# Kernel optimization log

Hardware: AMD Instinct MI355X
Metric: run time of the kernel (lower is better)

Reference implementation:

```python
import jax, jax.numpy as jnp
import numpy as np

B, T, DYN, STAT, H, OUT = 128, 2048, 8, 24, 256, 1

def setup_inputs() -> dict:
    key = jax.random.key(0)
    ks = jax.random.split(key, 20)
    s = lambda k, shape, fan_in: jax.random.uniform(k, shape, jnp.float32, -1.0, 1.0) / np.sqrt(fan_in)
    return {
        "x":    jax.random.normal(ks[0], (B, T, DYN + STAT), jnp.float32),
        "c0":   jax.random.normal(ks[1], (H,), jnp.float32),
        "h0":   jax.random.normal(ks[2], (H,), jnp.float32),
        "Wi":   s(ks[3], (H, STAT), STAT), "bi":   s(ks[4], (H,), STAT),
        "Wf_x": s(ks[5], (H, DYN), DYN),  "bf_x": s(ks[6], (H,), DYN),
        "Wf_h": s(ks[7], (H, H), H),      "bf_h": s(ks[8], (H,), H),
        "Wg_x": s(ks[9], (H, DYN), DYN),  "bg_x": s(ks[10], (H,), DYN),
        "Wg_h": s(ks[11], (H, H), H),     "bg_h": s(ks[12], (H,), H),
        "Wo_x": s(ks[13], (H, DYN), DYN), "bo_x": s(ks[14], (H,), DYN),
        "Wo_h": s(ks[15], (H, H), H),     "bo_h": s(ks[16], (H,), H),
        "Wout": s(ks[17], (OUT, H), H),   "bout": s(ks[18], (OUT,), H),
    }

def reference(x, c0, h0, Wi, bi, Wf_x, bf_x, Wf_h, bf_h,
              Wg_x, bg_x, Wg_h, bg_h, Wo_x, bo_x, Wo_h, bo_h, Wout, bout):
    xd = x[..., :DYN]   # [B,T,DYN] dynamic features
    xs = x[..., DYN:]   # [B,T,STAT] static features (recomputed each step, as in source)
    # Hoist all input-dependent gate pre-activations out of the recurrence.
    I  = jax.nn.sigmoid(jnp.einsum('btd,hd->bth', xs, Wi) + bi)   # input gate (static only)
    Fx = jnp.einsum('btd,hd->bth', xd, Wf_x) + bf_x
    Gx = jnp.einsum('btd,hd->bth', xd, Wg_x) + bg_x
    Ox = jnp.einsum('btd,hd->bth', xd, Wo_x) + bo_x

    def step(carry, inp):
        c, h = carry
        i_t, fx, gx, ox = inp
        f = jax.nn.sigmoid(fx + h @ Wf_h.T + bf_h)
        g = jnp.tanh(gx + h @ Wg_h.T + bg_h)
        o = jax.nn.sigmoid(ox + h @ Wo_h.T + bo_h)
        out = o @ Wout.T + bout          # NOTE: source computes output from o_t (pre-update)
        c = f * c + i_t * g
        h = o * jnp.tanh(c)
        return (c, h), out

    carry0 = (jnp.broadcast_to(c0, (B, H)), jnp.broadcast_to(h0, (B, H)))
    seq = (jnp.swapaxes(I, 0, 1), jnp.swapaxes(Fx, 0, 1),
           jnp.swapaxes(Gx, 0, 1), jnp.swapaxes(Ox, 0, 1))  # [T,B,H] each
    _, outs = jax.lax.scan(step, carry0, seq)
    return jnp.swapaxes(outs, 0, 1)  # [B,T,OUT]
```

## Files before the change

kernel.cpp:

```cpp
#include <hip/hip_runtime.h>
#include <hip/hip_bf16.h>


#define T_LEN 2048
#define HD 256

typedef __attribute__((ext_vector_type(8))) short bf16x8;
typedef __attribute__((ext_vector_type(4))) float f32x4;

#define LOG2E 1.4426950408889634f

__device__ __forceinline__ short f2bf(float f) {
  unsigned u = __float_as_uint(f);
  unsigned r = (u + 0x7fffu + ((u >> 16) & 1u)) >> 16;
  return (short)r;
}

__device__ __forceinline__ bf16x8 loadw8(const float* p) {
  bf16x8 r;
#pragma unroll
  for (int i = 0; i < 8; ++i) r[i] = f2bf(p[i]);
  return r;
}

__device__ __forceinline__ float sigm(float x) {
  float e = __builtin_amdgcn_exp2f(-LOG2E * x);
  return __builtin_amdgcn_rcpf(1.0f + e);
}

__device__ __forceinline__ float tanh_(float x) {
  float e = __builtin_amdgcn_exp2f((2.0f * LOG2E) * x);
  return 1.0f - 2.0f * __builtin_amdgcn_rcpf(e + 1.0f);
}

__device__ __forceinline__ void wg_barrier_lgkm() {
  asm volatile("s_waitcnt lgkmcnt(0)" ::: "memory");
  __builtin_amdgcn_s_barrier();
  __builtin_amdgcn_sched_barrier(0);
}

#define ASTR 296
#define ABUF (16 * ASTR)

__global__ __launch_bounds__(512, 2) void ealstm_kernel(
    const float* __restrict__ x, const float* __restrict__ c0, const float* __restrict__ h0,
    const float* __restrict__ Wi, const float* __restrict__ bi,
    const float* __restrict__ Wfx, const float* __restrict__ bfx,
    const float* __restrict__ Wfh, const float* __restrict__ bfh,
    const float* __restrict__ Wgx, const float* __restrict__ bgx,
    const float* __restrict__ Wgh, const float* __restrict__ bgh,
    const float* __restrict__ Wox, const float* __restrict__ box_,
    const float* __restrict__ Woh, const float* __restrict__ boh,
    const float* __restrict__ Wout, const float* __restrict__ bout,
    float* __restrict__ out)
{
  __shared__ __attribute__((aligned(16))) short A_sh[2 * ABUF];
  __shared__ __attribute__((aligned(16))) short Bx_sh[8 * 8 * 512];
  __shared__ __attribute__((aligned(16))) short Bo7_sh[8 * 2 * 512];
  __shared__ float out_part[2][4][32];

  const int tid = threadIdx.x;
  const int w   = tid >> 6;
  const int l   = tid & 63;
  const int lr  = l & 15;
  const int lg  = l >> 4;
  const int n0  = w * 32;
  const int wg  = blockIdx.x;
  const bool xstage = (tid >= 384);

  bf16x8 Bf[8][2], Bg[8][2], Bo[7][2];
#pragma unroll
  for (int ks = 0; ks < 8; ++ks) {
#pragma unroll
    for (int nt = 0; nt < 2; ++nt) {
      const int n = n0 + nt * 16 + lr;
      const int k = ks * 32 + lg * 8;
      Bf[ks][nt] = loadw8(Wfh + n * HD + k);
      Bg[ks][nt] = loadw8(Wgh + n * HD + k);
      if (ks < 7) Bo[ks][nt] = loadw8(Woh + n * HD + k);
    }
  }

  short* bo7 = Bo7_sh + w * 1024;
#pragma unroll
  for (int nt = 0; nt < 2; ++nt) {
    const int n = n0 + nt * 16 + lr;
    bf16x8 fr = loadw8(Woh + n * HD + 7 * 32 + lg * 8);
    *reinterpret_cast<bf16x8*>(bo7 + nt * 512 + l * 8) = fr;
  }
  short* bxw = Bx_sh + w * 4096;
  {
    bf16x8 z = (bf16x8)(short)0;
    const float* WxArr[3] = {Wfx, Wgx, Wox};
#pragma unroll
    for (int nt = 0; nt < 2; ++nt) {
      const int n = n0 + nt * 16 + lr;
#pragma unroll
      for (int g = 0; g < 3; ++g) {
        bf16x8 fr = (lg == 0) ? loadw8(WxArr[g] + n * 8) : z;
        *reinterpret_cast<bf16x8*>(bxw + (g * 2 + nt) * 512 + l * 8) = fr;
      }
      bf16x8 fi = (lg >= 1) ? loadw8(Wi + n * 24 + (lg - 1) * 8) : z;
      *reinterpret_cast<bf16x8*>(bxw + (6 + nt) * 512 + l * 8) = fi;
    }
  }

  float bias[4][2], woutv[2], cst[2];
#pragma unroll
  for (int nt = 0; nt < 2; ++nt) {
    const int n = n0 + nt * 16 + lr;
    bias[0][nt] = bfx[n] + bfh[n];
    bias[1][nt] = bgx[n] + bgh[n];
    bias[2][nt] = box_[n] + boh[n];
    bias[3][nt] = bi[n];
    woutv[nt] = Wout[n];
    cst[nt] = c0[n];
  }
  const float boutv = bout[0];

  for (int idx = tid; idx < 2 * ABUF; idx += 512) A_sh[idx] = 0;
  __syncthreads();
  for (int idx = tid; idx < 4 * 256; idx += 512) {
    A_sh[(4 * (idx >> 8)) * ASTR + (idx & 255)] = f2bf(h0[idx & 255]);
  }
  if (xstage) {
    const int row = (tid >> 5) & 3, k = tid & 31;
    A_sh[(4 * row) * ASTR + 256 + k] = f2bf(x[((size_t)(wg * 4 + row) * T_LEN) * 32 + k]);
  }
  __syncthreads();

  const float* xp = x + (size_t)(wg * 4 + ((tid >> 5) & 3)) * T_LEN * 32 + (tid & 31);
  const int akoff = lg * 8;
  const f32x4 z4 = {0.f, 0.f, 0.f, 0.f};

  for (int t = 0; t < T_LEN; ++t) {
    const int cur = t & 1;
    const short* ArowC = A_sh + cur * ABUF + lr * ASTR;
    short* Anxt = A_sh + (cur ^ 1) * ABUF;

    if (t > 0 && w == 0 && l < 4) {
      float s = boutv;
#pragma unroll
      for (int ww = 0; ww < 32; ++ww) s += out_part[cur ^ 1][l][ww];
      out[(size_t)(wg * 4 + l) * T_LEN + (t - 1)] = s;
    }

    float xval = 0.0f;
    if (xstage) {
      const int tn = (t + 1 < T_LEN) ? (t + 1) : (T_LEN - 1);
      xval = xp[(size_t)tn * 32];
    }

    f32x4 acc[4][2];
    const bf16x8 a0 = *reinterpret_cast<const bf16x8*>(ArowC + 0 * 32 + akoff);
    const bf16x8 a1 = *reinterpret_cast<const bf16x8*>(ArowC + 1 * 32 + akoff);
    const bf16x8 a2 = *reinterpret_cast<const bf16x8*>(ArowC + 2 * 32 + akoff);
    const bf16x8 a3 = *reinterpret_cast<const bf16x8*>(ArowC + 3 * 32 + akoff);
    __builtin_amdgcn_s_setprio(1);
    {
      acc[0][0] = __builtin_amdgcn_mfma_f32_16x16x32_bf16(a0, Bf[0][0], z4, 0, 0, 0);
      acc[0][1] = __builtin_amdgcn_mfma_f32_16x16x32_bf16(a0, Bf[0][1], z4, 0, 0, 0);
      acc[1][0] = __builtin_amdgcn_mfma_f32_16x16x32_bf16(a0, Bg[0][0], z4, 0, 0, 0);
      acc[1][1] = __builtin_amdgcn_mfma_f32_16x16x32_bf16(a0, Bg[0][1], z4, 0, 0, 0);
      acc[2][0] = __builtin_amdgcn_mfma_f32_16x16x32_bf16(a0, Bo[0][0], z4, 0, 0, 0);
      acc[2][1] = __builtin_amdgcn_mfma_f32_16x16x32_bf16(a0, Bo[0][1], z4, 0, 0, 0);
    }
    {
      const bf16x8 aa[3] = {a1, a2, a3};
#pragma unroll
      for (int ks = 1; ks < 4; ++ks) {
        const bf16x8 a = aa[ks - 1];
        acc[0][0] = __builtin_amdgcn_mfma_f32_16x16x32_bf16(a, Bf[ks][0], acc[0][0], 0, 0, 0);
        acc[0][1] = __builtin_amdgcn_mfma_f32_16x16x32_bf16(a, Bf[ks][1], acc[0][1], 0, 0, 0);
        acc[1][0] = __builtin_amdgcn_mfma_f32_16x16x32_bf16(a, Bg[ks][0], acc[1][0], 0, 0, 0);
        acc[1][1] = __builtin_amdgcn_mfma_f32_16x16x32_bf16(a, Bg[ks][1], acc[1][1], 0, 0, 0);
        acc[2][0] = __builtin_amdgcn_mfma_f32_16x16x32_bf16(a, Bo[ks][0], acc[2][0], 0, 0, 0);
        acc[2][1] = __builtin_amdgcn_mfma_f32_16x16x32_bf16(a, Bo[ks][1], acc[2][1], 0, 0, 0);
      }
    }
#pragma unroll
    for (int ks = 4; ks < 8; ++ks) {
      const bf16x8 a = *reinterpret_cast<const bf16x8*>(ArowC + ks * 32 + akoff);
      acc[0][0] = __builtin_amdgcn_mfma_f32_16x16x32_bf16(a, Bf[ks][0], acc[0][0], 0, 0, 0);
      acc[0][1] = __builtin_amdgcn_mfma_f32_16x16x32_bf16(a, Bf[ks][1], acc[0][1], 0, 0, 0);
      acc[1][0] = __builtin_amdgcn_mfma_f32_16x16x32_bf16(a, Bg[ks][0], acc[1][0], 0, 0, 0);
      acc[1][1] = __builtin_amdgcn_mfma_f32_16x16x32_bf16(a, Bg[ks][1], acc[1][1], 0, 0, 0);
      if (ks < 7) {
        acc[2][0] = __builtin_amdgcn_mfma_f32_16x16x32_bf16(a, Bo[ks][0], acc[2][0], 0, 0, 0);
        acc[2][1] = __builtin_amdgcn_mfma_f32_16x16x32_bf16(a, Bo[ks][1], acc[2][1], 0, 0, 0);
      } else {
        const bf16x8 b0 = *reinterpret_cast<const bf16x8*>(bo7 + 0 * 512 + l * 8);
        const bf16x8 b1 = *reinterpret_cast<const bf16x8*>(bo7 + 1 * 512 + l * 8);
        acc[2][0] = __builtin_amdgcn_mfma_f32_16x16x32_bf16(a, b0, acc[2][0], 0, 0, 0);
        acc[2][1] = __builtin_amdgcn_mfma_f32_16x16x32_bf16(a, b1, acc[2][1], 0, 0, 0);
      }
    }
    {
      const bf16x8 ax = *reinterpret_cast<const bf16x8*>(ArowC + 256 + akoff);
#pragma unroll
      for (int g = 0; g < 3; ++g) {
#pragma unroll
        for (int nt = 0; nt < 2; ++nt) {
          const bf16x8 b = *reinterpret_cast<const bf16x8*>(bxw + (g * 2 + nt) * 512 + l * 8);
          acc[g][nt] = __builtin_amdgcn_mfma_f32_16x16x32_bf16(ax, b, acc[g][nt], 0, 0, 0);
        }
      }
#pragma unroll
      for (int nt = 0; nt < 2; ++nt) {
        const bf16x8 b = *reinterpret_cast<const bf16x8*>(bxw + (6 + nt) * 512 + l * 8);
        f32x4 cb; cb[0] = bias[3][nt]; cb[1] = bias[3][nt]; cb[2] = bias[3][nt]; cb[3] = bias[3][nt];
        acc[3][nt] = __builtin_amdgcn_mfma_f32_16x16x32_bf16(ax, b, cb, 0, 0, 0);
      }
    }
    __builtin_amdgcn_s_setprio(0);

    float po = 0.0f;
    short hpk[2];
#pragma unroll
    for (int nt = 0; nt < 2; ++nt) {
      const float fpre = acc[0][nt][0] + bias[0][nt];
      const float gpre = acc[1][nt][0] + bias[1][nt];
      const float opre = acc[2][nt][0] + bias[2][nt];
      const float ipre = acc[3][nt][0];
      const float sf = sigm(fpre);
      const float tg = tanh_(gpre);
      const float so = sigm(opre);
      const float si = sigm(ipre);
      const float c  = sf * cst[nt] + si * tg;
      cst[nt] = c;
      const float hv = so * tanh_(c);
      hpk[nt] = f2bf(hv);
      po += so * woutv[nt];
    }

    Anxt[(4 * lg) * ASTR + (n0 + lr)]      = hpk[0];
    Anxt[(4 * lg) * ASTR + (n0 + 16 + lr)] = hpk[1];
    if (xstage) Anxt[(4 * ((tid >> 5) & 3)) * ASTR + 256 + (tid & 31)] = f2bf(xval);

    po += __shfl_xor(po, 1, 64);
    po += __shfl_xor(po, 2, 64);
    if ((lr & 3) == 0) out_part[cur][lg][w * 4 + (lr >> 2)] = po;

    wg_barrier_lgkm();
  }

  if (w == 0 && l < 4) {
    float s = boutv;
#pragma unroll
    for (int ww = 0; ww < 32; ++ww) s += out_part[(T_LEN - 1) & 1][l][ww];
    out[(size_t)(wg * 4 + l) * T_LEN + (T_LEN - 1)] = s;
  }
}

extern "C" void kernel_launch(void* const* d_in, const int* in_sizes, int n_in,
                              void* d_out, int out_size, void* d_ws, size_t ws_size,
                              hipStream_t stream) {
  const float* x    = (const float*)d_in[0];
  const float* c0   = (const float*)d_in[1];
  const float* h0   = (const float*)d_in[2];
  const float* Wi   = (const float*)d_in[3];
  const float* bi   = (const float*)d_in[4];
  const float* Wfx  = (const float*)d_in[5];
  const float* bfx  = (const float*)d_in[6];
  const float* Wfh  = (const float*)d_in[7];
  const float* bfh  = (const float*)d_in[8];
  const float* Wgx  = (const float*)d_in[9];
  const float* bgx  = (const float*)d_in[10];
  const float* Wgh  = (const float*)d_in[11];
  const float* bgh  = (const float*)d_in[12];
  const float* Wox  = (const float*)d_in[13];
  const float* box_ = (const float*)d_in[14];
  const float* Woh  = (const float*)d_in[15];
  const float* boh  = (const float*)d_in[16];
  const float* Wout = (const float*)d_in[17];
  const float* bout = (const float*)d_in[18];

  ealstm_kernel<<<dim3(32), dim3(512), 0, stream>>>(
      x, c0, h0, Wi, bi, Wfx, bfx, Wfh, bfh,
      Wgx, bgx, Wgh, bgh, Wox, box_, Woh, boh, Wout, bout,
      (float*)d_out);
}
```

Before: 2.806 ms.

## Precompute input-gate pre-activations in chunks to workspace before recurrence

Adds a new kernel that, per time chunk, runs a batched MFMA pass over x to compute the input-projection gate pre-activations (with biases and sigmoid of the input gate). It stores them as packed bf16 in the workspace, and the recurrent loop then reads them through a two-step-ahead register prefetch. This removes the per-step x MFMAs, the x staging into shared memory and the associated extra A-tile columns from the serial critical path. In exchange it adds global round-trips and rounds the gate pre-activations to bf16. It falls back to the old kernel when the workspace is too small.

```diff
diff --git a/kernel.cpp b/kernel.cpp
--- a/kernel.cpp
+++ b/kernel.cpp
@@ -7,6 +7,7 @@
 
 typedef __attribute__((ext_vector_type(8))) short bf16x8;
 typedef __attribute__((ext_vector_type(4))) float f32x4;
+typedef __attribute__((ext_vector_type(4))) unsigned int u32x4;
 
 #define LOG2E 1.4426950408889634f
 
@@ -23,6 +24,15 @@
   return r;
 }
 
+__device__ __forceinline__ bf16x8 loadw8v(const float* p) {
+  const float4 v0 = *reinterpret_cast<const float4*>(p);
+  const float4 v1 = *reinterpret_cast<const float4*>(p + 4);
+  bf16x8 r;
+  r[0] = f2bf(v0.x); r[1] = f2bf(v0.y); r[2] = f2bf(v0.z); r[3] = f2bf(v0.w);
+  r[4] = f2bf(v1.x); r[5] = f2bf(v1.y); r[6] = f2bf(v1.z); r[7] = f2bf(v1.w);
+  return r;
+}
+
 __device__ __forceinline__ float sigm(float x) {
   float e = __builtin_amdgcn_exp2f(-LOG2E * x);
   return __builtin_amdgcn_rcpf(1.0f + e);
@@ -31,6 +41,11 @@
 __device__ __forceinline__ float tanh_(float x) {
   float e = __builtin_amdgcn_exp2f((2.0f * LOG2E) * x);
   return 1.0f - 2.0f * __builtin_amdgcn_rcpf(e + 1.0f);
+}
+
+__device__ __forceinline__ float punp16(u32x4 p, int idx) {
+  unsigned d = p[idx >> 1];
+  return __uint_as_float((idx & 1) ? (d & 0xffff0000u) : (d << 16));
 }
 
 __device__ __forceinline__ void wg_barrier_lgkm() {
@@ -39,10 +54,230 @@
   __builtin_amdgcn_sched_barrier(0);
 }
 
-#define ASTR 296
+#define ASTR 264
 #define ABUF (16 * ASTR)
 
-__global__ __launch_bounds__(512, 2) void ealstm_kernel(
+__global__ __launch_bounds__(512, 2) void ealstm_pp(
+    const float* __restrict__ x, const float* __restrict__ c0, const float* __restrict__ h0,
+    const float* __restrict__ Wi, const float* __restrict__ bi,
+    const float* __restrict__ Wfx, const float* __restrict__ bfx,
+    const float* __restrict__ Wfh, const float* __restrict__ bfh,
+    const float* __restrict__ Wgx, const float* __restrict__ bgx,
+    const float* __restrict__ Wgh, const float* __restrict__ bgh,
+    const float* __restrict__ Wox, const float* __restrict__ box_,
+    const float* __restrict__ Woh, const float* __restrict__ boh,
+    const float* __restrict__ Wout, const float* __restrict__ bout,
+    float* __restrict__ out, unsigned short* __restrict__ P, int tc)
+{
+  __shared__ __attribute__((aligned(16))) short A_sh[2 * ABUF];
+  __shared__ __attribute__((aligned(16))) short Bo7_sh[8 * 2 * 512];
+  __shared__ float out_part[2][4][32];
+
+  const int tid = threadIdx.x;
+  const int w   = tid >> 6;
+  const int l   = tid & 63;
+  const int lr  = l & 15;
+  const int lg  = l >> 4;
+  const int n0  = w * 32;
+  const int wg  = blockIdx.x;
+
+  bf16x8 Bw[4][2];
+  float cb[4][2];
+  {
+    bf16x8 z = (bf16x8)(short)0;
+#pragma unroll
+    for (int nt = 0; nt < 2; ++nt) {
+      const int n = n0 + nt * 16 + lr;
+      Bw[0][nt] = (lg == 0) ? loadw8(Wfx + n * 8) : z;
+      Bw[1][nt] = (lg == 0) ? loadw8(Wgx + n * 8) : z;
+      Bw[2][nt] = (lg == 0) ? loadw8(Wox + n * 8) : z;
+      Bw[3][nt] = (lg >= 1) ? loadw8(Wi + n * 24 + (lg - 1) * 8) : z;
+      cb[0][nt] = bfx[n] + bfh[n];
+      cb[1][nt] = bgx[n] + bgh[n];
+      cb[2][nt] = box_[n] + boh[n];
+      cb[3][nt] = bi[n];
+    }
+  }
+
+  bf16x8 Bf[8][2], Bg[8][2], Bo[7][2];
+#pragma unroll
+  for (int ks = 0; ks < 8; ++ks) {
+#pragma unroll
+    for (int nt = 0; nt < 2; ++nt) {
+      const int n = n0 + nt * 16 + lr;
+      const int k = ks * 32 + lg * 8;
+      Bf[ks][nt] = loadw8(Wfh + n * HD + k);
+      Bg[ks][nt] = loadw8(Wgh + n * HD + k);
+      if (ks < 7) Bo[ks][nt] = loadw8(Woh + n * HD + k);
+    }
+  }
+  short* bo7 = Bo7_sh + w * 1024;
+#pragma unroll
+  for (int nt = 0; nt < 2; ++nt) {
+    const int n = n0 + nt * 16 + lr;
+    bf16x8 fr = loadw8(Woh + n * HD + 7 * 32 + lg * 8);
+    *reinterpret_cast<bf16x8*>(bo7 + nt * 512 + l * 8) = fr;
+  }
+
+  float woutv[2], cst[2];
+#pragma unroll
+  for (int nt = 0; nt < 2; ++nt) {
+    const int n = n0 + nt * 16 + lr;
+    woutv[nt] = Wout[n];
+    cst[nt]   = c0[n];
+  }
+  const float boutv = bout[0];
+
+  for (int idx = tid; idx < 2 * ABUF; idx += 512) A_sh[idx] = 0;
+  __syncthreads();
+  for (int idx = tid; idx < 4 * 256; idx += 512) {
+    A_sh[(4 * (idx >> 8)) * ASTR + (idx & 255)] = f2bf(h0[idx & 255]);
+  }
+  __syncthreads();
+
+  unsigned short* Pw = P + ((size_t)wg * 8 + w) * ((size_t)tc * 512);
+  const unsigned short* Pr = Pw + ((size_t)lg * 16 + lr) * 8;
+  const int akoff = lg * 8;
+  const f32x4 z4 = {0.f, 0.f, 0.f, 0.f};
+
+  for (int t0c = 0; t0c < T_LEN; t0c += tc) {
+    const int ntiles = tc >> 2;
+#pragma unroll 1
+    for (int tile = 0; tile < ntiles; ++tile) {
+      const int row  = tile & 3;
+      const int trow = (tile >> 2) << 4;
+      const float* xr = x + ((size_t)(wg * 4 + row) * T_LEN + t0c + trow + lr) * 32 + akoff;
+      const bf16x8 a = loadw8v(xr);
+      f32x4 acc[4][2];
+#pragma unroll
+      for (int g = 0; g < 4; ++g) {
+#pragma unroll
+        for (int nt = 0; nt < 2; ++nt) {
+          f32x4 cbs; cbs[0] = cb[g][nt]; cbs[1] = cb[g][nt]; cbs[2] = cb[g][nt]; cbs[3] = cb[g][nt];
+          acc[g][nt] = __builtin_amdgcn_mfma_f32_16x16x32_bf16(a, Bw[g][nt], cbs, 0, 0, 0);
+        }
+      }
+#pragma unroll
+      for (int r = 0; r < 4; ++r) {
+        bf16x8 pk;
+        pk[0] = f2bf(acc[0][0][r]); pk[1] = f2bf(acc[0][1][r]);
+        pk[2] = f2bf(acc[1][0][r]); pk[3] = f2bf(acc[1][1][r]);
+        pk[4] = f2bf(acc[2][0][r]); pk[5] = f2bf(acc[2][1][r]);
+        pk[6] = f2bf(sigm(acc[3][0][r])); pk[7] = f2bf(sigm(acc[3][1][r]));
+        *reinterpret_cast<bf16x8*>(Pw + ((size_t)(trow + lg * 4 + r) * 4 + row) * 128 + lr * 8) = pk;
+      }
+    }
+    asm volatile("s_waitcnt vmcnt(0)" ::: "memory");
+
+    u32x4 pc = *reinterpret_cast<const u32x4*>(Pr);
+    u32x4 pn = *reinterpret_cast<const u32x4*>(Pr + ((tc > 1) ? 512 : 0));
+
+#pragma unroll 1
+    for (int tl = 0; tl < tc; ++tl) {
+      const int t   = t0c + tl;
+      const int cur = t & 1;
+      const short* ArowC = A_sh + cur * ABUF + lr * ASTR;
+      short* Anxt = A_sh + (cur ^ 1) * ABUF;
+
+      const int t2 = (tl + 2 < tc) ? (tl + 2) : (tc - 1);
+      const u32x4 p2 = *reinterpret_cast<const u32x4*>(Pr + (size_t)t2 * 512);
+
+      if (t > 0 && w == 0 && l < 4) {
+        float s = boutv;
+#pragma unroll
+        for (int ww = 0; ww < 32; ++ww) s += out_part[cur ^ 1][l][ww];
+        out[(size_t)(wg * 4 + l) * T_LEN + (t - 1)] = s;
+      }
+
+      f32x4 acc[3][2];
+      const bf16x8 a0 = *reinterpret_cast<const bf16x8*>(ArowC + 0 * 32 + akoff);
+      const bf16x8 a1 = *reinterpret_cast<const bf16x8*>(ArowC + 1 * 32 + akoff);
+      const bf16x8 a2 = *reinterpret_cast<const bf16x8*>(ArowC + 2 * 32 + akoff);
+      const bf16x8 a3 = *reinterpret_cast<const bf16x8*>(ArowC + 3 * 32 + akoff);
+      __builtin_amdgcn_s_setprio(1);
+      {
+        acc[0][0] = __builtin_amdgcn_mfma_f32_16x16x32_bf16(a0, Bf[0][0], z4, 0, 0, 0);
+        acc[0][1] = __builtin_amdgcn_mfma_f32_16x16x32_bf16(a0, Bf[0][1], z4, 0, 0, 0);
+        acc[1][0] = __builtin_amdgcn_mfma_f32_16x16x32_bf16(a0, Bg[0][0], z4, 0, 0, 0);
+        acc[1][1] = __builtin_amdgcn_mfma_f32_16x16x32_bf16(a0, Bg[0][1], z4, 0, 0, 0);
+        acc[2][0] = __builtin_amdgcn_mfma_f32_16x16x32_bf16(a0, Bo[0][0], z4, 0, 0, 0);
+        acc[2][1] = __builtin_amdgcn_mfma_f32_16x16x32_bf16(a0, Bo[0][1], z4, 0, 0, 0);
+      }
+      {
+        const bf16x8 aa[3] = {a1, a2, a3};
+#pragma unroll
+        for (int ks = 1; ks < 4; ++ks) {
+          const bf16x8 a = aa[ks - 1];
+          acc[0][0] = __builtin_amdgcn_mfma_f32_16x16x32_bf16(a, Bf[ks][0], acc[0][0], 0, 0, 0);
+          acc[0][1] = __builtin_amdgcn_mfma_f32_16x16x32_bf16(a, Bf[ks][1], acc[0][1], 0, 0, 0);
+          acc[1][0] = __builtin_amdgcn_mfma_f32_16x16x32_bf16(a, Bg[ks][0], acc[1][0], 0, 0, 0);
+          acc[1][1] = __builtin_amdgcn_mfma_f32_16x16x32_bf16(a, Bg[ks][1], acc[1][1], 0, 0, 0);
+          acc[2][0] = __builtin_amdgcn_mfma_f32_16x16x32_bf16(a, Bo[ks][0], acc[2][0], 0, 0, 0);
+          acc[2][1] = __builtin_amdgcn_mfma_f32_16x16x32_bf16(a, Bo[ks][1], acc[2][1], 0, 0, 0);
+        }
+      }
+#pragma unroll
+      for (int ks = 4; ks < 8; ++ks) {
+        const bf16x8 a = *reinterpret_cast<const bf16x8*>(ArowC + ks * 32 + akoff);
+        acc[0][0] = __builtin_amdgcn_mfma_f32_16x16x32_bf16(a, Bf[ks][0], acc[0][0], 0, 0, 0);
+        acc[0][1] = __builtin_amdgcn_mfma_f32_16x16x32_bf16(a, Bf[ks][1], acc[0][1], 0, 0, 0);
+        acc[1][0] = __builtin_amdgcn_mfma_f32_16x16x32_bf16(a, Bg[ks][0], acc[1][0], 0, 0, 0);
+        acc[1][1] = __builtin_amdgcn_mfma_f32_16x16x32_bf16(a, Bg[ks][1], acc[1][1], 0, 0, 0);
+        if (ks < 7) {
+          acc[2][0] = __builtin_amdgcn_mfma_f32_16x16x32_bf16(a, Bo[ks][0], acc[2][0], 0, 0, 0);
+          acc[2][1] = __builtin_amdgcn_mfma_f32_16x16x32_bf16(a, Bo[ks][1], acc[2][1], 0, 0, 0);
+        } else {
+          const bf16x8 b0 = *reinterpret_cast<const bf16x8*>(bo7 + 0 * 512 + l * 8);
+          const bf16x8 b1 = *reinterpret_cast<const bf16x8*>(bo7 + 1 * 512 + l * 8);
+          acc[2][0] = __builtin_amdgcn_mfma_f32_16x16x32_bf16(a, b0, acc[2][0], 0, 0, 0);
+          acc[2][1] = __builtin_amdgcn_mfma_f32_16x16x32_bf16(a, b1, acc[2][1], 0, 0, 0);
+        }
+      }
+      __builtin_amdgcn_s_setprio(0);
+
+      float po = 0.0f;
+      short hpk[2];
+#pragma unroll
+      for (int nt = 0; nt < 2; ++nt) {
+        const float fpre = acc[0][nt][0] + punp16(pc, 0 + nt);
+        const float gpre = acc[1][nt][0] + punp16(pc, 2 + nt);
+        const float opre = acc[2][nt][0] + punp16(pc, 4 + nt);
+        const float si   = punp16(pc, 6 + nt);
+        const float sf = sigm(fpre);
+        const float tg = tanh_(gpre);
+        const float so = sigm(opre);
+        const float c  = sf * cst[nt] + si * tg;
+        cst[nt] = c;
+        const float hv = so * tanh_(c);
+        hpk[nt] = f2bf(hv);
+        po += so * woutv[nt];
+      }
+
+      Anxt[(4 * lg) * ASTR + (n0 + lr)]      = hpk[0];
+      Anxt[(4 * lg) * ASTR + (n0 + 16 + lr)] = hpk[1];
+
+      po += __shfl_xor(po, 1, 64);
+      po += __shfl_xor(po, 2, 64);
+      if ((lr & 3) == 0) out_part[cur][lg][w * 4 + (lr >> 2)] = po;
+
+      pc = pn; pn = p2;
+
+      wg_barrier_lgkm();
+    }
+  }
+
+  if (w == 0 && l < 4) {
+    float s = boutv;
+#pragma unroll
+    for (int ww = 0; ww < 32; ++ww) s += out_part[(T_LEN - 1) & 1][l][ww];
+    out[(size_t)(wg * 4 + l) * T_LEN + (T_LEN - 1)] = s;
+  }
+}
+
+#define FASTR 296
+#define FABUF (16 * FASTR)
+
+__global__ __launch_bounds__(512, 2) void ealstm_fb(
     const float* __restrict__ x, const float* __restrict__ c0, const float* __restrict__ h0,
     const float* __restrict__ Wi, const float* __restrict__ bi,
     const float* __restrict__ Wfx, const float* __restrict__ bfx,
@@ -54,7 +289,7 @@
     const float* __restrict__ Wout, const float* __restrict__ bout,
     float* __restrict__ out)
 {
-  __shared__ __attribute__((aligned(16))) short A_sh[2 * ABUF];
+  __shared__ __attribute__((aligned(16))) short A_sh[2 * FABUF];
   __shared__ __attribute__((aligned(16))) short Bx_sh[8 * 8 * 512];
   __shared__ __attribute__((aligned(16))) short Bo7_sh[8 * 2 * 512];
   __shared__ float out_part[2][4][32];
@@ -80,7 +315,6 @@
       if (ks < 7) Bo[ks][nt] = loadw8(Woh + n * HD + k);
     }
   }
-
   short* bo7 = Bo7_sh + w * 1024;
 #pragma unroll
   for (int nt = 0; nt < 2; ++nt) {
@@ -118,14 +352,14 @@
   }
   const float boutv = bout[0];
 
-  for (int idx = tid; idx < 2 * ABUF; idx += 512) A_sh[idx] = 0;
+  for (int idx = tid; idx < 2 * FABUF; idx += 512) A_sh[idx] = 0;
   __syncthreads();
   for (int idx = tid; idx < 4 * 256; idx += 512) {
-    A_sh[(4 * (idx >> 8)) * ASTR + (idx & 255)] = f2bf(h0[idx & 255]);
+    A_sh[(4 * (idx >> 8)) * FASTR + (idx & 255)] = f2bf(h0[idx & 255]);
   }
   if (xstage) {
     const int row = (tid >> 5) & 3, k = tid & 31;
-    A_sh[(4 * row) * ASTR + 256 + k] = f2bf(x[((size_t)(wg * 4 + row) * T_LEN) * 32 + k]);
+    A_sh[(4 * row) * FASTR + 256 + k] = f2bf(x[((size_t)(wg * 4 + row) * T_LEN) * 32 + k]);
   }
   __syncthreads();
 
@@ -135,8 +369,8 @@
 
   for (int t = 0; t < T_LEN; ++t) {
     const int cur = t & 1;
-    const short* ArowC = A_sh + cur * ABUF + lr * ASTR;
-    short* Anxt = A_sh + (cur ^ 1) * ABUF;
+    const short* ArowC = A_sh + cur * FABUF + lr * FASTR;
+    short* Anxt = A_sh + (cur ^ 1) * FABUF;
 
     if (t > 0 && w == 0 && l < 4) {
       float s = boutv;
@@ -208,8 +442,8 @@
 #pragma unroll
       for (int nt = 0; nt < 2; ++nt) {
         const bf16x8 b = *reinterpret_cast<const bf16x8*>(bxw + (6 + nt) * 512 + l * 8);
-        f32x4 cb; cb[0] = bias[3][nt]; cb[1] = bias[3][nt]; cb[2] = bias[3][nt]; cb[3] = bias[3][nt];
-        acc[3][nt] = __builtin_amdgcn_mfma_f32_16x16x32_bf16(ax, b, cb, 0, 0, 0);
+        f32x4 cbv; cbv[0] = bias[3][nt]; cbv[1] = bias[3][nt]; cbv[2] = bias[3][nt]; cbv[3] = bias[3][nt];
+        acc[3][nt] = __builtin_amdgcn_mfma_f32_16x16x32_bf16(ax, b, cbv, 0, 0, 0);
       }
     }
     __builtin_amdgcn_s_setprio(0);
@@ -233,9 +467,9 @@
       po += so * woutv[nt];
     }
 
-    Anxt[(4 * lg) * ASTR + (n0 + lr)]      = hpk[0];
-    Anxt[(4 * lg) * ASTR + (n0 + 16 + lr)] = hpk[1];
-    if (xstage) Anxt[(4 * ((tid >> 5) & 3)) * ASTR + 256 + (tid & 31)] = f2bf(xval);
+    Anxt[(4 * lg) * FASTR + (n0 + lr)]      = hpk[0];
+    Anxt[(4 * lg) * FASTR + (n0 + 16 + lr)] = hpk[1];
+    if (xstage) Anxt[(4 * ((tid >> 5) & 3)) * FASTR + 256 + (tid & 31)] = f2bf(xval);
 
     po += __shfl_xor(po, 1, 64);
     po += __shfl_xor(po, 2, 64);
@@ -275,8 +509,20 @@
   const float* Wout = (const float*)d_in[17];
   const float* bout = (const float*)d_in[18];
 
-  ealstm_kernel<<<dim3(32), dim3(512), 0, stream>>>(
-      x, c0, h0, Wi, bi, Wfx, bfx, Wfh, bfh,
-      Wgx, bgx, Wgh, bgh, Wox, box_, Woh, boh, Wout, bout,
-      (float*)d_out);
-}
+  int tc = 0;
+  for (int cand = T_LEN; cand >= 64; cand >>= 1) {
+    if (ws_size >= (size_t)cand * 262144) { tc = cand; break; }
+  }
+
+  if (tc) {
+    ealstm_pp<<<dim3(32), dim3(512), 0, stream>>>(
+        x, c0, h0, Wi, bi, Wfx, bfx, Wfh, bfh,
+        Wgx, bgx, Wgh, bgh, Wox, box_, Woh, boh, Wout, bout,
+        (float*)d_out, (unsigned short*)d_ws, tc);
+  } else {
+    ealstm_fb<<<dim3(32), dim3(512), 0, stream>>>(
+        x, c0, h0, Wi, bi, Wfx, bfx, Wfh, bfh,
+        Wgx, bgx, Wgh, bgh, Wox, box_, Woh, boh, Wout, bout,
+        (float*)d_out);
+  }
+}
```

New measurement: 6.514 ms. +132.2%, slower.

## Batch input-gate projections over 8-step chunks and drop x from recurrent MFMA

Applied to the files above, without the earlier changes.

Every 8 timesteps, the 8 upcoming x rows per batch are loaded and their input projections (f, g, o, and the sigmoid input gate) are computed as full 16-row MFMA tiles. The results are packed to bf16 and stored in per-wave LDS. The per-step recurrent loop then only runs the h-dependent MFMAs and reads the precomputed pre-activations, instead of doing 8 extra x MFMAs with mostly zero rows every step. This is meant to shorten the serial per-step critical path and drop the per-step x staging into LDS. The cost is an occasional chunk-compute burst, and extra rounding because the input pre-activations and biases are stored in bf16.

```diff
diff --git a/kernel.cpp b/kernel.cpp
--- a/kernel.cpp
+++ b/kernel.cpp
@@ -7,6 +7,7 @@
 
 typedef __attribute__((ext_vector_type(8))) short bf16x8;
 typedef __attribute__((ext_vector_type(4))) float f32x4;
+typedef __attribute__((ext_vector_type(4))) unsigned int u32x4;
 
 #define LOG2E 1.4426950408889634f
 
@@ -23,6 +24,13 @@
   return r;
 }
 
+__device__ __forceinline__ bf16x8 cvt8(float4 a, float4 b) {
+  bf16x8 r;
+  r[0] = f2bf(a.x); r[1] = f2bf(a.y); r[2] = f2bf(a.z); r[3] = f2bf(a.w);
+  r[4] = f2bf(b.x); r[5] = f2bf(b.y); r[6] = f2bf(b.z); r[7] = f2bf(b.w);
+  return r;
+}
+
 __device__ __forceinline__ float sigm(float x) {
   float e = __builtin_amdgcn_exp2f(-LOG2E * x);
   return __builtin_amdgcn_rcpf(1.0f + e);
@@ -31,6 +39,11 @@
 __device__ __forceinline__ float tanh_(float x) {
   float e = __builtin_amdgcn_exp2f((2.0f * LOG2E) * x);
   return 1.0f - 2.0f * __builtin_amdgcn_rcpf(e + 1.0f);
+}
+
+__device__ __forceinline__ float punp16(u32x4 p, int idx) {
+  unsigned d = p[idx >> 1];
+  return __uint_as_float((idx & 1) ? (d & 0xffff0000u) : (d << 16));
 }
 
 __device__ __forceinline__ void wg_barrier_lgkm() {
@@ -39,7 +52,7 @@
   __builtin_amdgcn_sched_barrier(0);
 }
 
-#define ASTR 296
+#define ASTR 264
 #define ABUF (16 * ASTR)
 
 __global__ __launch_bounds__(512, 2) void ealstm_kernel(
@@ -55,8 +68,8 @@
     float* __restrict__ out)
 {
   __shared__ __attribute__((aligned(16))) short A_sh[2 * ABUF];
-  __shared__ __attribute__((aligned(16))) short Bx_sh[8 * 8 * 512];
   __shared__ __attribute__((aligned(16))) short Bo7_sh[8 * 2 * 512];
+  __shared__ __attribute__((aligned(16))) short P_sh[8 * 8 * 512];
   __shared__ float out_part[2][4][32];
 
   const int tid = threadIdx.x;
@@ -66,7 +79,24 @@
   const int lg  = l >> 4;
   const int n0  = w * 32;
   const int wg  = blockIdx.x;
-  const bool xstage = (tid >= 384);
+
+  bf16x8 Bw[4][2];
+  float cb[4][2];
+  {
+    bf16x8 z = (bf16x8)(short)0;
+#pragma unroll
+    for (int nt = 0; nt < 2; ++nt) {
+      const int n = n0 + nt * 16 + lr;
+      Bw[0][nt] = (lg == 0) ? loadw8(Wfx + n * 8) : z;
+      Bw[1][nt] = (lg == 0) ? loadw8(Wgx + n * 8) : z;
+      Bw[2][nt] = (lg == 0) ? loadw8(Wox + n * 8) : z;
+      Bw[3][nt] = (lg >= 1) ? loadw8(Wi + n * 24 + (lg - 1) * 8) : z;
+      cb[0][nt] = bfx[n] + bfh[n];
+      cb[1][nt] = bgx[n] + bgh[n];
+      cb[2][nt] = box_[n] + boh[n];
+      cb[3][nt] = bi[n];
+    }
+  }
 
   bf16x8 Bf[8][2], Bg[8][2], Bo[7][2];
 #pragma unroll
@@ -80,7 +110,6 @@
       if (ks < 7) Bo[ks][nt] = loadw8(Woh + n * HD + k);
     }
   }
-
   short* bo7 = Bo7_sh + w * 1024;
 #pragma unroll
   for (int nt = 0; nt < 2; ++nt) {
@@ -88,33 +117,13 @@
     bf16x8 fr = loadw8(Woh + n * HD + 7 * 32 + lg * 8);
     *reinterpret_cast<bf16x8*>(bo7 + nt * 512 + l * 8) = fr;
   }
-  short* bxw = Bx_sh + w * 4096;
-  {
-    bf16x8 z = (bf16x8)(short)0;
-    const float* WxArr[3] = {Wfx, Wgx, Wox};
-#pragma unroll
-    for (int nt = 0; nt < 2; ++nt) {
-      const int n = n0 + nt * 16 + lr;
-#pragma unroll
-      for (int g = 0; g < 3; ++g) {
-        bf16x8 fr = (lg == 0) ? loadw8(WxArr[g] + n * 8) : z;
-        *reinterpret_cast<bf16x8*>(bxw + (g * 2 + nt) * 512 + l * 8) = fr;
-      }
-      bf16x8 fi = (lg >= 1) ? loadw8(Wi + n * 24 + (lg - 1) * 8) : z;
-      *reinterpret_cast<bf16x8*>(bxw + (6 + nt) * 512 + l * 8) = fi;
-    }
-  }
-
-  float bias[4][2], woutv[2], cst[2];
+
+  float woutv[2], cst[2];
 #pragma unroll
   for (int nt = 0; nt < 2; ++nt) {
     const int n = n0 + nt * 16 + lr;
-    bias[0][nt] = bfx[n] + bfh[n];
-    bias[1][nt] = bgx[n] + bgh[n];
-    bias[2][nt] = box_[n] + boh[n];
-    bias[3][nt] = bi[n];
     woutv[nt] = Wout[n];
-    cst[nt] = c0[n];
+    cst[nt]   = c0[n];
   }
   const float boutv = bout[0];
 
@@ -123,125 +132,145 @@
   for (int idx = tid; idx < 4 * 256; idx += 512) {
     A_sh[(4 * (idx >> 8)) * ASTR + (idx & 255)] = f2bf(h0[idx & 255]);
   }
-  if (xstage) {
-    const int row = (tid >> 5) & 3, k = tid & 31;
-    A_sh[(4 * row) * ASTR + 256 + k] = f2bf(x[((size_t)(wg * 4 + row) * T_LEN) * 32 + k]);
-  }
   __syncthreads();
 
-  const float* xp = x + (size_t)(wg * 4 + ((tid >> 5) & 3)) * T_LEN * 32 + (tid & 31);
+  short* Pl = P_sh + w * 4096;
   const int akoff = lg * 8;
   const f32x4 z4 = {0.f, 0.f, 0.f, 0.f};
 
-  for (int t = 0; t < T_LEN; ++t) {
-    const int cur = t & 1;
-    const short* ArowC = A_sh + cur * ABUF + lr * ASTR;
-    short* Anxt = A_sh + (cur ^ 1) * ABUF;
-
-    if (t > 0 && w == 0 && l < 4) {
-      float s = boutv;
-#pragma unroll
-      for (int ww = 0; ww < 32; ++ww) s += out_part[cur ^ 1][l][ww];
-      out[(size_t)(wg * 4 + l) * T_LEN + (t - 1)] = s;
+  const size_t xoff0 = ((size_t)(wg * 4 + 0 + (lr >> 3)) * T_LEN + (lr & 7)) * 32 + akoff;
+  const size_t xoff1 = ((size_t)(wg * 4 + 2 + (lr >> 3)) * T_LEN + (lr & 7)) * 32 + akoff;
+
+  float4 xbuf[4];
+  xbuf[0] = *reinterpret_cast<const float4*>(x + xoff0);
+  xbuf[1] = *reinterpret_cast<const float4*>(x + xoff0 + 4);
+  xbuf[2] = *reinterpret_cast<const float4*>(x + xoff1);
+  xbuf[3] = *reinterpret_cast<const float4*>(x + xoff1 + 4);
+
+  for (int t0c = 0; t0c < T_LEN; t0c += 8) {
+    {
+      const bf16x8 aT0 = cvt8(xbuf[0], xbuf[1]);
+      const bf16x8 aT1 = cvt8(xbuf[2], xbuf[3]);
+      const size_t tnoff = (size_t)((t0c + 8 < T_LEN) ? (t0c + 8) : t0c) * 32;
+      xbuf[0] = *reinterpret_cast<const float4*>(x + xoff0 + tnoff);
+      xbuf[1] = *reinterpret_cast<const float4*>(x + xoff0 + tnoff + 4);
+      xbuf[2] = *reinterpret_cast<const float4*>(x + xoff1 + tnoff);
+      xbuf[3] = *reinterpret_cast<const float4*>(x + xoff1 + tnoff + 4);
+
+      const bf16x8 aTs[2] = {aT0, aT1};
+#pragma unroll
+      for (int tile = 0; tile < 2; ++tile) {
+        f32x4 pacc[4][2];
+#pragma unroll
+        for (int g = 0; g < 4; ++g) {
+#pragma unroll
+          for (int nt = 0; nt < 2; ++nt) {
+            f32x4 cbs; cbs[0] = cb[g][nt]; cbs[1] = cb[g][nt]; cbs[2] = cb[g][nt]; cbs[3] = cb[g][nt];
+            pacc[g][nt] = __builtin_amdgcn_mfma_f32_16x16x32_bf16(aTs[tile], Bw[g][nt], cbs, 0, 0, 0);
+          }
+        }
+#pragma unroll
+        for (int r = 0; r < 4; ++r) {
+          const int mq = lg * 4 + r;
+          bf16x8 pk;
+          pk[0] = f2bf(pacc[0][0][r]); pk[1] = f2bf(pacc[0][1][r]);
+          pk[2] = f2bf(pacc[1][0][r]); pk[3] = f2bf(pacc[1][1][r]);
+          pk[4] = f2bf(pacc[2][0][r]); pk[5] = f2bf(pacc[2][1][r]);
+          pk[6] = f2bf(sigm(pacc[3][0][r])); pk[7] = f2bf(sigm(pacc[3][1][r]));
+          *reinterpret_cast<bf16x8*>(Pl + (mq & 7) * 512 + (tile * 2 + (mq >> 3)) * 128 + lr * 8) = pk;
+        }
+      }
     }
 
-    float xval = 0.0f;
-    if (xstage) {
-      const int tn = (t + 1 < T_LEN) ? (t + 1) : (T_LEN - 1);
-      xval = xp[(size_t)tn * 32];
-    }
-
-    f32x4 acc[4][2];
-    const bf16x8 a0 = *reinterpret_cast<const bf16x8*>(ArowC + 0 * 32 + akoff);
-    const bf16x8 a1 = *reinterpret_cast<const bf16x8*>(ArowC + 1 * 32 + akoff);
-    const bf16x8 a2 = *reinterpret_cast<const bf16x8*>(ArowC + 2 * 32 + akoff);
-    const bf16x8 a3 = *reinterpret_cast<const bf16x8*>(ArowC + 3 * 32 + akoff);
-    __builtin_amdgcn_s_setprio(1);
-    {
-      acc[0][0] = __builtin_amdgcn_mfma_f32_16x16x32_bf16(a0, Bf[0][0], z4, 0, 0, 0);
-      acc[0][1] = __builtin_amdgcn_mfma_f32_16x16x32_bf16(a0, Bf[0][1], z4, 0, 0, 0);
-      acc[1][0] = __builtin_amdgcn_mfma_f32_16x16x32_bf16(a0, Bg[0][0], z4, 0, 0, 0);
-      acc[1][1] = __builtin_amdgcn_mfma_f32_16x16x32_bf16(a0, Bg[0][1], z4, 0, 0, 0);
-      acc[2][0] = __builtin_amdgcn_mfma_f32_16x16x32_bf16(a0, Bo[0][0], z4, 0, 0, 0);
-      acc[2][1] = __builtin_amdgcn_mfma_f32_16x16x32_bf16(a0, Bo[0][1], z4, 0, 0, 0);
-    }
-    {
-      const bf16x8 aa[3] = {a1, a2, a3};
-#pragma unroll
-      for (int ks = 1; ks < 4; ++ks) {
-        const bf16x8 a = aa[ks - 1];
+#pragma unroll 1
+    for (int tl = 0; tl < 8; ++tl) {
+      const int t   = t0c + tl;
+      const int cur = t & 1;
+      const short* ArowC = A_sh + cur * ABUF + lr * ASTR;
+      short* Anxt = A_sh + (cur ^ 1) * ABUF;
+
+      const u32x4 pc = *reinterpret_cast<const u32x4*>(Pl + tl * 512 + lg * 128 + lr * 8);
+
+      if (t > 0 && w == 0 && l < 4) {
+        float s = boutv;
+#pragma unroll
+        for (int ww = 0; ww < 32; ++ww) s += out_part[cur ^ 1][l][ww];
+        out[(size_t)(wg * 4 + l) * T_LEN + (t - 1)] = s;
+      }
+
+      f32x4 acc[3][2];
+      const bf16x8 a0 = *reinterpret_cast<const bf16x8*>(ArowC + 0 * 32 + akoff);
+      const bf16x8 a1 = *reinterpret_cast<const bf16x8*>(ArowC + 1 * 32 + akoff);
+      const bf16x8 a2 = *reinterpret_cast<const bf16x8*>(ArowC + 2 * 32 + akoff);
+      const bf16x8 a3 = *reinterpret_cast<const bf16x8*>(ArowC + 3 * 32 + akoff);
+      __builtin_amdgcn_s_setprio(1);
+      {
+        acc[0][0] = __builtin_amdgcn_mfma_f32_16x16x32_bf16(a0, Bf[0][0], z4, 0, 0, 0);
+        acc[0][1] = __builtin_amdgcn_mfma_f32_16x16x32_bf16(a0, Bf[0][1], z4, 0, 0, 0);
+        acc[1][0] = __builtin_amdgcn_mfma_f32_16x16x32_bf16(a0, Bg[0][0], z4, 0, 0, 0);
+        acc[1][1] = __builtin_amdgcn_mfma_f32_16x16x32_bf16(a0, Bg[0][1], z4, 0, 0, 0);
+        acc[2][0] = __builtin_amdgcn_mfma_f32_16x16x32_bf16(a0, Bo[0][0], z4, 0, 0, 0);
+        acc[2][1] = __builtin_amdgcn_mfma_f32_16x16x32_bf16(a0, Bo[0][1], z4, 0, 0, 0);
+      }
+      {
+        const bf16x8 aa[3] = {a1, a2, a3};
+#pragma unroll
+        for (int ks = 1; ks < 4; ++ks) {
+          const bf16x8 a = aa[ks - 1];
+          acc[0][0] = __builtin_amdgcn_mfma_f32_16x16x32_bf16(a, Bf[ks][0], acc[0][0], 0, 0, 0);
+          acc[0][1] = __builtin_amdgcn_mfma_f32_16x16x32_bf16(a, Bf[ks][1], acc[0][1], 0, 0, 0);
+          acc[1][0] = __builtin_amdgcn_mfma_f32_16x16x32_bf16(a, Bg[ks][0], acc[1][0], 0, 0, 0);
+          acc[1][1] = __builtin_amdgcn_mfma_f32_16x16x32_bf16(a, Bg[ks][1], acc[1][1], 0, 0, 0);
+          acc[2][0] = __builtin_amdgcn_mfma_f32_16x16x32_bf16(a, Bo[ks][0], acc[2][0], 0, 0, 0);
+          acc[2][1] = __builtin_amdgcn_mfma_f32_16x16x32_bf16(a, Bo[ks][1], acc[2][1], 0, 0, 0);
+        }
+      }
+#pragma unroll
+      for (int ks = 4; ks < 8; ++ks) {
+        const bf16x8 a = *reinterpret_cast<const bf16x8*>(ArowC + ks * 32 + akoff);
         acc[0][0] = __builtin_amdgcn_mfma_f32_16x16x32_bf16(a, Bf[ks][0], acc[0][0], 0, 0, 0);
         acc[0][1] = __builtin_amdgcn_mfma_f32_16x16x32_bf16(a, Bf[ks][1], acc[0][1], 0, 0, 0);
         acc[1][0] = __builtin_amdgcn_mfma_f32_16x16x32_bf16(a, Bg[ks][0], acc[1][0], 0, 0, 0);
         acc[1][1] = __builtin_amdgcn_mfma_f32_16x16x32_bf16(a, Bg[ks][1], acc[1][1], 0, 0, 0);
-        acc[2][0] = __builtin_amdgcn_mfma_f32_16x16x32_bf16(a, Bo[ks][0], acc[2][0], 0, 0, 0);
-        acc[2][1] = __builtin_amdgcn_mfma_f32_16x16x32_bf16(a, Bo[ks][1], acc[2][1], 0, 0, 0);
-      }
+        if (ks < 7) {
+          acc[2][0] = __builtin_amdgcn_mfma_f32_16x16x32_bf16(a, Bo[ks][0], acc[2][0], 0, 0, 0);
+          acc[2][1] = __builtin_amdgcn_mfma_f32_16x16x32_bf16(a, Bo[ks][1], acc[2][1], 0, 0, 0);
+        } else {
+          const bf16x8 b0 = *reinterpret_cast<const bf16x8*>(bo7 + 0 * 512 + l * 8);
+          const bf16x8 b1 = *reinterpret_cast<const bf16x8*>(bo7 + 1 * 512 + l * 8);
+          acc[2][0] = __builtin_amdgcn_mfma_f32_16x16x32_bf16(a, b0, acc[2][0], 0, 0, 0);
+          acc[2][1] = __builtin_amdgcn_mfma_f32_16x16x32_bf16(a, b1, acc[2][1], 0, 0, 0);
+        }
+      }
+      __builtin_amdgcn_s_setprio(0);
+
+      float po = 0.0f;
+      short hpk[2];
+#pragma unroll
+      for (int nt = 0; nt < 2; ++nt) {
+        const float fpre = acc[0][nt][0] + punp16(pc, 0 + nt);
+        const float gpre = acc[1][nt][0] + punp16(pc, 2 + nt);
+        const float opre = acc[2][nt][0] + punp16(pc, 4 + nt);
+        const float si   = punp16(pc, 6 + nt);
+        const float sf = sigm(fpre);
+        const float tg = tanh_(gpre);
+        const float so = sigm(opre);
+        const float c  = sf * cst[nt] + si * tg;
+        cst[nt] = c;
+        const float hv = so * tanh_(c);
+        hpk[nt] = f2bf(hv);
+        po += so * woutv[nt];
+      }
+
+      Anxt[(4 * lg) * ASTR + (n0 + lr)]      = hpk[0];
+      Anxt[(4 * lg) * ASTR + (n0 + 16 + lr)] = hpk[1];
+
+      po += __shfl_xor(po, 1, 64);
+      po += __shfl_xor(po, 2, 64);
+      if ((lr & 3) == 0) out_part[cur][lg][w * 4 + (lr >> 2)] = po;
+
+      wg_barrier_lgkm();
     }
-#pragma unroll
-    for (int ks = 4; ks < 8; ++ks) {
-      const bf16x8 a = *reinterpret_cast<const bf16x8*>(ArowC + ks * 32 + akoff);
-      acc[0][0] = __builtin_amdgcn_mfma_f32_16x16x32_bf16(a, Bf[ks][0], acc[0][0], 0, 0, 0);
-      acc[0][1] = __builtin_amdgcn_mfma_f32_16x16x32_bf16(a, Bf[ks][1], acc[0][1], 0, 0, 0);
-      acc[1][0] = __builtin_amdgcn_mfma_f32_16x16x32_bf16(a, Bg[ks][0], acc[1][0], 0, 0, 0);
-      acc[1][1] = __builtin_amdgcn_mfma_f32_16x16x32_bf16(a, Bg[ks][1], acc[1][1], 0, 0, 0);
-      if (ks < 7) {
-        acc[2][0] = __builtin_amdgcn_mfma_f32_16x16x32_bf16(a, Bo[ks][0], acc[2][0], 0, 0, 0);
-        acc[2][1] = __builtin_amdgcn_mfma_f32_16x16x32_bf16(a, Bo[ks][1], acc[2][1], 0, 0, 0);
-      } else {
-        const bf16x8 b0 = *reinterpret_cast<const bf16x8*>(bo7 + 0 * 512 + l * 8);
-        const bf16x8 b1 = *reinterpret_cast<const bf16x8*>(bo7 + 1 * 512 + l * 8);
-        acc[2][0] = __builtin_amdgcn_mfma_f32_16x16x32_bf16(a, b0, acc[2][0], 0, 0, 0);
-        acc[2][1] = __builtin_amdgcn_mfma_f32_16x16x32_bf16(a, b1, acc[2][1], 0, 0, 0);
-      }
-    }
-    {
-      const bf16x8 ax = *reinterpret_cast<const bf16x8*>(ArowC + 256 + akoff);
-#pragma unroll
-      for (int g = 0; g < 3; ++g) {
-#pragma unroll
-        for (int nt = 0; nt < 2; ++nt) {
-          const bf16x8 b = *reinterpret_cast<const bf16x8*>(bxw + (g * 2 + nt) * 512 + l * 8);
-          acc[g][nt] = __builtin_amdgcn_mfma_f32_16x16x32_bf16(ax, b, acc[g][nt], 0, 0, 0);
-        }
-      }
-#pragma unroll
-      for (int nt = 0; nt < 2; ++nt) {
-        const bf16x8 b = *reinterpret_cast<const bf16x8*>(bxw + (6 + nt) * 512 + l * 8);
-        f32x4 cb; cb[0] = bias[3][nt]; cb[1] = bias[3][nt]; cb[2] = bias[3][nt]; cb[3] = bias[3][nt];
-        acc[3][nt] = __builtin_amdgcn_mfma_f32_16x16x32_bf16(ax, b, cb, 0, 0, 0);
-      }
-    }
-    __builtin_amdgcn_s_setprio(0);
-
-    float po = 0.0f;
-    short hpk[2];
-#pragma unroll
-    for (int nt = 0; nt < 2; ++nt) {
-      const float fpre = acc[0][nt][0] + bias[0][nt];
-      const float gpre = acc[1][nt][0] + bias[1][nt];
-      const float opre = acc[2][nt][0] + bias[2][nt];
-      const float ipre = acc[3][nt][0];
-      const float sf = sigm(fpre);
-      const float tg = tanh_(gpre);
-      const float so = sigm(opre);
-      const float si = sigm(ipre);
-      const float c  = sf * cst[nt] + si * tg;
-      cst[nt] = c;
-      const float hv = so * tanh_(c);
-      hpk[nt] = f2bf(hv);
-      po += so * woutv[nt];
-    }
-
-    Anxt[(4 * lg) * ASTR + (n0 + lr)]      = hpk[0];
-    Anxt[(4 * lg) * ASTR + (n0 + 16 + lr)] = hpk[1];
-    if (xstage) Anxt[(4 * ((tid >> 5) & 3)) * ASTR + 256 + (tid & 31)] = f2bf(xval);
-
-    po += __shfl_xor(po, 1, 64);
-    po += __shfl_xor(po, 2, 64);
-    if ((lr & 3) == 0) out_part[cur][lg][w * 4 + (lr >> 2)] = po;
-
-    wg_barrier_lgkm();
   }
 
   if (w == 0 && l < 4) {
```

New measurement: 4.662 ms. 66.1% more time.
